# Kernel tuning notes

Measured on AMD Instinct MI355X. Metric: run time of the kernel, lower is better.

The kernel has to match this reference:

```python
import jax, jax.numpy as jnp
import numpy as np

D_MODEL = 384; D_INNER = 768; D_STATE = 64; D_CONV = 4
HEADDIM = 48; NHEADS = 16; NLAYERS = 2
VOCAB = 4104  # 4098 (4096 6-mers + PAD/UNK) padded to multiple of 8
B, L = 32, 512
D_IN_PROJ = 2 * D_INNER + 2 * D_STATE + NHEADS  # 1664
CONV_DIM = D_INNER + 2 * D_STATE  # 896
N_ORDER, N_FAMILY, N_GENUS, N_SPECIES = 60, 427, 14216, 23964


def _layernorm(x, w, b, eps=1e-5):
    mu = jnp.mean(x, -1, keepdims=True)
    var = jnp.mean((x - mu) ** 2, -1, keepdims=True)
    return (x - mu) * jax.lax.rsqrt(var + eps) * w + b


def _mamba2(h, W_in, cw, cb, dtb, alog, d_skip, gw, W_out):
    b, l, _ = h.shape
    zxbcdt = h @ W_in                                  # (b,l,1664)
    z = zxbcdt[..., :D_INNER]
    xBC = zxbcdt[..., D_INNER:D_INNER + CONV_DIM]
    dt = zxbcdt[..., -NHEADS:]
    # causal depthwise conv1d (kernel D_CONV) + silu
    xp = jnp.pad(xBC, ((0, 0), (D_CONV - 1, 0), (0, 0)))
    conv = cb + sum(xp[:, k:k + l, :] * cw[:, k] for k in range(D_CONV))
    xBC = jax.nn.silu(conv)
    x = xBC[..., :D_INNER].reshape(b, l, NHEADS, HEADDIM)
    Bm = xBC[..., D_INNER:D_INNER + D_STATE]           # (b,l,n) ngroups=1
    Cm = xBC[..., D_INNER + D_STATE:]
    dt = jax.nn.softplus(dt + dtb)                     # (b,l,h)
    dA = jnp.exp(dt * (-jnp.exp(alog)))                # per-head scalar decay
    tm = lambda a: jnp.swapaxes(a, 0, 1)               # time-major for scan

    def step(state, inp):
        xt, dtt, dAt, Bt, Ct = inp                     # (b,h,p),(b,h),(b,h),(b,n),(b,n)
        state = state * dAt[:, :, None, None] + jnp.einsum('bhp,bn->bhpn', dtt[..., None] * xt, Bt)
        return state, jnp.einsum('bhpn,bn->bhp', state, Ct)

    state0 = jnp.zeros((b, NHEADS, HEADDIM, D_STATE), h.dtype)
    _, ys = jax.lax.scan(step, state0, (tm(x), tm(dt), tm(dA), tm(Bm), tm(Cm)))
    y = tm(ys) + d_skip[None, None, :, None] * x       # D skip per head
    y = y.reshape(b, l, D_INNER) * jax.nn.silu(z)      # gate
    y = y * jax.lax.rsqrt(jnp.mean(y * y, -1, keepdims=True) + 1e-5) * gw  # gated RMSNorm
    return y @ W_out


def setup_inputs():
    key = jax.random.key(0)
    ks = jax.random.split(key, 16)
    nrm = lambda k, s, sc=0.02: jax.random.normal(k, s, jnp.float32) * sc
    return {
        'tokens': jax.random.randint(ks[0], (B, L), 0, VOCAB),
        'emb': nrm(ks[1], (VOCAB, D_MODEL)),
        'ln_w': jnp.ones((NLAYERS, D_MODEL)), 'ln_b': jnp.zeros((NLAYERS, D_MODEL)),
        'in_proj_w': nrm(ks[2], (NLAYERS, D_MODEL, D_IN_PROJ)),
        'conv_w': nrm(ks[3], (NLAYERS, CONV_DIM, D_CONV), 0.1),
        'conv_b': jnp.zeros((NLAYERS, CONV_DIM)),
        'dt_bias': nrm(ks[4], (NLAYERS, NHEADS), 0.5),
        'A_log': jnp.log(jax.random.uniform(ks[5], (NLAYERS, NHEADS), minval=1.0, maxval=16.0)),
        'D': jnp.ones((NLAYERS, NHEADS)),
        'gnorm_w': jnp.ones((NLAYERS, D_INNER)),
        'out_proj_w': nrm(ks[6], (NLAYERS, D_INNER, D_MODEL)),
        'normf_w': jnp.ones((D_MODEL,)), 'normf_b': jnp.zeros((D_MODEL,)),
        'proj_ln_w': jnp.ones((D_MODEL,)), 'proj_ln_b': jnp.zeros((D_MODEL,)),
        'order_w': nrm(ks[7], (D_MODEL, N_ORDER)), 'order_b': jnp.zeros((N_ORDER,)),
        'family_w': nrm(ks[8], (D_MODEL, N_FAMILY)), 'family_b': jnp.zeros((N_FAMILY,)),
        'genus_w': nrm(ks[9], (D_MODEL, N_GENUS)), 'genus_b': jnp.zeros((N_GENUS,)),
        'species_w': nrm(ks[10], (D_MODEL, N_SPECIES)), 'species_b': jnp.zeros((N_SPECIES,)),
    }


def reference(tokens, emb, ln_w, ln_b, in_proj_w, conv_w, conv_b, dt_bias, A_log, D, gnorm_w, out_proj_w, normf_w, normf_b, proj_ln_w, proj_ln_b, order_w, order_b, family_w, family_b, genus_w, genus_b, species_w, species_b):
    resid = emb[tokens]                                # (B,L,d), embed dropout off (eval)
    for l in range(NLAYERS):                           # pre-norm residual blocks
        h = _layernorm(resid, ln_w[l], ln_b[l])
        resid = resid + _mamba2(h, in_proj_w[l], conv_w[l], conv_b[l], dt_bias[l], A_log[l], D[l], gnorm_w[l], out_proj_w[l])
    h = _layernorm(resid, normf_w, normf_b)            # norm_f -> hidden states
    feat = _layernorm(h.mean(axis=1), proj_ln_w, proj_ln_b)  # mean pool + shared LN (dropout eval)
    return jnp.concatenate([feat @ order_w + order_b,
                            feat @ family_w + family_b,
                            feat @ genus_w + genus_b,
                            feat @ species_w + species_b], axis=-1)
```

## Files before the change

kernel.cpp:

```cpp
#include <hip/hip_runtime.h>
#include <hip/hip_bf16.h>
#include <cmath>


#define B_SZ 32
#define L_SZ 512
#define DMODEL 384
#define DINNER 768
#define DSTATE 64
#define HEADDIM 48
#define NHEADS 16
#define DINPROJ 1680
#define CONVDIM 896
#define ROWS (B_SZ * L_SZ)
#define OUT_STRIDE 38667
#define NCH 8
#define CHL (L_SZ / NCH)
#define N1PAD 1792
#define BCOFF 1536

typedef __hip_bfloat16 bf16;
typedef unsigned short u16;
typedef __attribute__((ext_vector_type(8))) short bfrag;
typedef __attribute__((ext_vector_type(4))) float ffrag;

union BU { uint4 u; bfrag f; };

__device__ __forceinline__ float ldw(const void* p, size_t i, bool isb) {
    if (isb) return __bfloat162float(((const bf16*)p)[i]);
    else     return ((const float*)p)[i];
}

__device__ __forceinline__ short f2bs(float f) {
    unsigned u = __float_as_uint(f);
    u = u + 0x7FFFu + ((u >> 16) & 1u);
    return (short)(u >> 16);
}
__device__ __forceinline__ unsigned pk2(float a, float b) {
    return ((unsigned)(u16)f2bs(a)) | (((unsigned)(u16)f2bs(b)) << 16);
}
__device__ __forceinline__ float blo(unsigned u) { return __uint_as_float(u << 16); }
__device__ __forceinline__ float bhi(unsigned u) { return __uint_as_float(u & 0xFFFF0000u); }

__device__ __forceinline__ void gl2lds16(const void* g, void* l) {
    __builtin_amdgcn_global_load_lds(
        (const __attribute__((address_space(1))) void*)g,
        (__attribute__((address_space(3))) void*)l, 16, 0, 0);
}

__device__ __forceinline__ float* send_f(float* zxd, int s, int off) {
    int seg = off / 768, rem = off - seg * 768;
    return zxd + (size_t)(4 * s + seg) * DINPROJ + DINNER + rem;
}
__device__ __forceinline__ float4* send_q(float* zxd, int s, int off4) {
    return (float4*)send_f(zxd, s, off4);
}

__global__ void detect_kernel(const void* __restrict__ ln_w, int* __restrict__ flag) {
    unsigned u = *(const unsigned*)ln_w;
    *flag = (u == 0x3F800000u) ? 0 : 1;
}

__global__ void embed_kernel(const int* __restrict__ tok,
                             const void* __restrict__ emb,
                             float* __restrict__ resid,
                             const int* __restrict__ dflag) {
    bool isb = (*dflag != 0);
    int r = blockIdx.x, d = threadIdx.x;
    resid[(size_t)r * DMODEL + d] = ldw(emb, (size_t)tok[r] * DMODEL + d, isb);
}

__global__ void layernorm_off(const float* __restrict__ x,
                              const void* __restrict__ w,
                              const void* __restrict__ b, long off,
                              void* __restrict__ out, int D, int obf,
                              const int* __restrict__ dflag) {
    bool isb = (*dflag != 0);
    int row = blockIdx.x, lane = threadIdx.x;
    const float* xr = x + (size_t)row * D;
    float s = 0.f, s2 = 0.f;
    for (int d = lane; d < D; d += 64) { float v = xr[d]; s += v; s2 += v * v; }
    #pragma unroll
    for (int o = 32; o; o >>= 1) { s += __shfl_xor(s, o); s2 += __shfl_xor(s2, o); }
    float mu = s / D;
    float var = s2 / D - mu * mu;
    float rinv = rsqrtf(var + 1e-5f);
    for (int d = lane; d < D; d += 64) {
        float v = (xr[d] - mu) * rinv * ldw(w, off + d, isb) + ldw(b, off + d, isb);
        if (obf) ((u16*)out)[(size_t)row * D + d] = (u16)f2bs(v);
        else     ((float*)out)[(size_t)row * D + d] = v;
    }
}

__global__ void transpose_w(const void* __restrict__ W, long woff,
                            int K, int N, u16* __restrict__ WT, int NT,
                            const int* __restrict__ dflag) {
    bool isb = (*dflag != 0);
    __shared__ float t[64][65];
    int n0 = blockIdx.x * 64, k0 = blockIdx.y * 64;
    for (int i = threadIdx.x; i < 4096; i += 256) {
        int kk = i >> 6, nn = i & 63;
        int gk = k0 + kk, gn = n0 + nn;
        float v = (gn < N && gk < K) ? ldw(W, woff + (size_t)gk * N + gn, isb) : 0.f;
        t[nn][kk] = v;
    }
    __syncthreads();
    for (int i = threadIdx.x; i < 4096; i += 256) {
        int nn = i >> 6, kk = i & 63;
        int gn = n0 + nn, gk = k0 + kk;
        if (gn < NT && gk < K)
            WT[(size_t)gn * K + gk] = (u16)f2bs(t[nn][kk]);
    }
}

__global__ __launch_bounds__(256)
void gemm128(const u16* __restrict__ A, int lda,
             const u16* __restrict__ BT, int ldb,
             float* __restrict__ C, int ldc,
             const float* __restrict__ Cadd,
             int N, int K) {
    __shared__ u16 As[128 * 64];
    __shared__ u16 Bs[128 * 64];
    const int tid = threadIdx.x, lane = tid & 63, w = tid >> 6;
    const int bm = blockIdx.y * 128, bn = blockIdx.x * 128;
    const int wr = w >> 1, wc = w & 1;
    ffrag acc[4][4];
    #pragma unroll
    for (int i = 0; i < 4; ++i)
        #pragma unroll
        for (int j = 0; j < 4; ++j) acc[i][j] = 0.f;

    const int sr = lane >> 3;
    const int swz = (((lane & 7) ^ sr) << 4) >> 1;
    const u16* Asrc = A + (size_t)bm * lda + swz;
    const u16* Bsrc = BT + (size_t)bn * ldb + swz;

    for (int k0 = 0; k0 < K; k0 += 64) {
        #pragma unroll
        for (int i = 0; i < 4; ++i) {
            int r = w * 32 + i * 8 + sr;
            gl2lds16(Asrc + (size_t)r * lda + k0, &As[(w * 32 + i * 8) * 64]);
            gl2lds16(Bsrc + (size_t)r * ldb + k0, &Bs[(w * 32 + i * 8) * 64]);
        }
        __syncthreads();
        #pragma unroll
        for (int ks = 0; ks < 2; ++ks) {
            bfrag af[4], bf[4];
            #pragma unroll
            for (int mi = 0; mi < 4; ++mi) {
                int rr = wr * 64 + mi * 16 + (lane & 15);
                int byte = (rr * 128 + ks * 64 + (lane >> 4) * 16) ^ ((rr & 7) << 4);
                af[mi] = *(const bfrag*)&As[byte >> 1];
            }
            #pragma unroll
            for (int ni = 0; ni < 4; ++ni) {
                int rr = wc * 64 + ni * 16 + (lane & 15);
                int byte = (rr * 128 + ks * 64 + (lane >> 4) * 16) ^ ((rr & 7) << 4);
                bf[ni] = *(const bfrag*)&Bs[byte >> 1];
            }
            #pragma unroll
            for (int mi = 0; mi < 4; ++mi)
                #pragma unroll
                for (int ni = 0; ni < 4; ++ni)
                    acc[mi][ni] = __builtin_amdgcn_mfma_f32_16x16x32_bf16(
                        af[mi], bf[ni], acc[mi][ni], 0, 0, 0);
        }
        __syncthreads();
    }
    int col = lane & 15, r0 = (lane >> 4) * 4;
    #pragma unroll
    for (int mi = 0; mi < 4; ++mi)
        #pragma unroll
        for (int ni = 0; ni < 4; ++ni) {
            int gn = bn + wc * 64 + ni * 16 + col;
            if (gn < N) {
                #pragma unroll
                for (int r = 0; r < 4; ++r) {
                    int gm = bm + wr * 64 + mi * 16 + r0 + r;
                    size_t idx = (size_t)gm * ldc + gn;
                    float v = acc[mi][ni][r];
                    if (Cadd) v += Cadd[idx];
                    C[idx] = v;
                }
            }
        }
}

__global__ void conv_silu_off(const float* __restrict__ zx,
                              const void* __restrict__ cw,
                              const void* __restrict__ cb,
                              long cwoff, long cboff,
                              float* __restrict__ out,
                              const int* __restrict__ dflag) {
    bool isb = (*dflag != 0);
    int c = blockIdx.x * 128 + threadIdx.x;
    int r = blockIdx.y;
    int l = r & (L_SZ - 1);
    float acc = ldw(cb, cboff + c, isb);
    #pragma unroll
    for (int k = 0; k < 4; ++k) {
        int lsrc = l + k - 3;
        if (lsrc >= 0)
            acc += zx[(size_t)(r + k - 3) * DINPROJ + DINNER + c] *
                   ldw(cw, cwoff + c * 4 + k, isb);
    }
    out[(size_t)r * CONVDIM + c] = acc / (1.f + expf(-acc));
}

__global__ __launch_bounds__(256)
void xpose(const float* __restrict__ cbuf, u16* __restrict__ xT) {
    int slot = blockIdx.x, tid = threadIdx.x;
    const float* src = cbuf + (size_t)slot * 64 * CONVDIM;
    u16* dst = xT + (size_t)slot * 49152;
    for (int it = 0; it < 24; ++it) {
        int p = (it % 3) * 256 + tid;
        int tg = it / 3;
        const float* s0 = src + (size_t)(tg * 8) * CONVDIM + p;
        uint4 pk;
        pk.x = pk2(s0[0],           s0[CONVDIM]);
        pk.y = pk2(s0[2 * CONVDIM], s0[3 * CONVDIM]);
        pk.z = pk2(s0[4 * CONVDIM], s0[5 * CONVDIM]);
        pk.w = pk2(s0[6 * CONVDIM], s0[7 * CONVDIM]);
        *(uint4*)(dst + tg * 6144 + p * 8) = pk;
    }
}

__global__ void dt_off(float* __restrict__ zx,
                       const float* __restrict__ convb,
                       const void* __restrict__ dtb,
                       long hoff,
                       float* __restrict__ dtout,
                       const int* __restrict__ dflag) {
    bool isb = (*dflag != 0);
    int idx = blockIdx.x * 256 + threadIdx.x;
    int r = idx >> 4, h = idx & 15;
    float x = zx[(size_t)r * DINPROJ + (DINPROJ - NHEADS) + h] + ldw(dtb, hoff + h, isb);
    float sp = (x > 20.f) ? x : log1pf(expf(x));
    dtout[idx] = sp;
    const float* cv = convb + (size_t)r * CONVDIM + DINNER + h * 8;
    float4 v0 = *(const float4*)cv;
    float4 v1 = *(const float4*)(cv + 4);
    uint4 pk;
    pk.x = pk2(v0.x, v0.y);
    pk.y = pk2(v0.z, v0.w);
    pk.z = pk2(v1.x, v1.y);
    pk.w = pk2(v1.z, v1.w);
    *(uint4*)((u16*)(zx + (size_t)r * DINPROJ + BCOFF) + h * 8) = pk;
}


__global__ __launch_bounds__(512)
void scan_p1(const float* __restrict__ dtg,
             const void* __restrict__ alog, long hoff,
             const u16* __restrict__ xT,
             float* __restrict__ zxd, float* __restrict__ Pbuf,
             const int* __restrict__ dflag) {
    bool isb = (*dflag != 0);
    int c = blockIdx.x & (NCH - 1);
    int hg = (blockIdx.x >> 3) & 1;
    int b = blockIdx.x >> 4;
    int lane = threadIdx.x & 63;
    int wv = threadIdx.x >> 6;
    int h = hg * 8 + wv;
    int slotC = b * NCH + c;
    int slotS = (b << 7) | (h << 3) | c;
    __shared__ __align__(16) u16 BT[64][72];
    __shared__ __align__(16) float La[8][64];
    __shared__ __align__(16) float Dt[8][64];
    #pragma unroll
    for (int it = 0; it < 8; ++it) {
        int idx = it * 512 + threadIdx.x;
        int t = idx >> 6, n = idx & 63;
        BT[n][t] = *((const u16*)(zxd + (size_t)(slotC * 64 + t) * DINPROJ + BCOFF) + n);
    }
    float dtv = dtg[((size_t)slotC * 64 + lane) * NHEADS + h];
    float A = expf(ldw(alog, hoff + h, isb));
    float cs = dtv;
    #pragma unroll
    for (int o = 1; o < 64; o <<= 1) { float v = __shfl_up(cs, o); if (lane >= o) cs += v; }
    La[wv][lane] = -A * cs;
    Dt[wv][lane] = dtv;
    __syncthreads();
    float la63 = La[wv][63];
    ffrag acc[3][4];
    #pragma unroll
    for (int i = 0; i < 3; ++i)
        #pragma unroll
        for (int j = 0; j < 4; ++j) acc[i][j] = 0.f;
    #pragma unroll
    for (int ks = 0; ks < 2; ++ks) {
        int t0 = ks * 32 + (lane >> 4) * 8;
        float4 lA = *(const float4*)&La[wv][t0];
        float4 lB = *(const float4*)&La[wv][t0 + 4];
        float4 dA4 = *(const float4*)&Dt[wv][t0];
        float4 dB4 = *(const float4*)&Dt[wv][t0 + 4];
        float v0 = expf(la63 - lA.x) * dA4.x;
        float v1 = expf(la63 - lA.y) * dA4.y;
        float v2 = expf(la63 - lA.z) * dA4.z;
        float v3 = expf(la63 - lA.w) * dA4.w;
        float v4 = expf(la63 - lB.x) * dB4.x;
        float v5 = expf(la63 - lB.y) * dB4.y;
        float v6 = expf(la63 - lB.z) * dB4.z;
        float v7 = expf(la63 - lB.w) * dB4.w;
        BU xv[3];
        #pragma unroll
        for (int ni = 0; ni < 3; ++ni) {
            int p = h * 48 + (lane & 15) + 16 * ni;
            uint4 raw = *(const uint4*)(xT + (size_t)slotC * 49152 + (t0 >> 3) * 6144 + p * 8);
            xv[ni].u.x = pk2(blo(raw.x) * v0, bhi(raw.x) * v1);
            xv[ni].u.y = pk2(blo(raw.y) * v2, bhi(raw.y) * v3);
            xv[ni].u.z = pk2(blo(raw.z) * v4, bhi(raw.z) * v5);
            xv[ni].u.w = pk2(blo(raw.w) * v6, bhi(raw.w) * v7);
        }
        #pragma unroll
        for (int nj = 0; nj < 4; ++nj) {
            bfrag bt = *(const bfrag*)&BT[(lane & 15) + 16 * nj][t0];
            #pragma unroll
            for (int mi = 0; mi < 3; ++mi)
                acc[mi][nj] = __builtin_amdgcn_mfma_f32_16x16x32_bf16(
                    xv[mi].f, bt, acc[mi][nj], 0, 0, 0);
        }
    }
    #pragma unroll
    for (int mi = 0; mi < 3; ++mi)
        #pragma unroll
        for (int nj = 0; nj < 4; ++nj)
            #pragma unroll
            for (int r = 0; r < 4; ++r) {
                int p = 16 * mi + (lane >> 4) * 4 + r;
                int n = 16 * nj + (lane & 15);
                *send_f(zxd, slotS, p * 64 + n) = acc[mi][nj][r];
            }
    if (lane == 0) Pbuf[slotS] = expf(la63);
}

__global__ void scan_p2(float* __restrict__ zxd, const float* __restrict__ Pbuf) {
    int bh = blockIdx.x;
    int lane = threadIdx.x;
    float4 S[12];
    #pragma unroll
    for (int q = 0; q < 12; ++q) S[q] = make_float4(0.f, 0.f, 0.f, 0.f);
    for (int c = 0; c < NCH - 1; ++c) {
        int s = bh * NCH + c;
        float P = Pbuf[s];
        #pragma unroll
        for (int q = 0; q < 12; ++q) {
            float4* p = send_q(zxd, s, 4 * lane + 256 * q);
            float4 L = *p;
            S[q].x = S[q].x * P + L.x;
            S[q].y = S[q].y * P + L.y;
            S[q].z = S[q].z * P + L.z;
            S[q].w = S[q].w * P + L.w;
            *p = S[q];
        }
    }
}

__global__ __launch_bounds__(512)
void scan_p3(float* __restrict__ convb,
             const float* __restrict__ dtg,
             const void* __restrict__ alog,
             const void* __restrict__ Dsk, long hoff,
             const u16* __restrict__ xT,
             float* __restrict__ zxd,
             const int* __restrict__ dflag) {
    bool isb = (*dflag != 0);
    int c = blockIdx.x & (NCH - 1);
    int hg = (blockIdx.x >> 3) & 1;
    int b = blockIdx.x >> 4;
    int lane = threadIdx.x & 63;
    int wv = threadIdx.x >> 6;
    int h = hg * 8 + wv;
    int slotC = b * NCH + c;
    int slotS = (b << 7) | (h << 3) | c;
    __shared__ __align__(16) u16 Bl[64][72];
    __shared__ __align__(16) u16 Cl[64][72];
    __shared__ __align__(16) float Gl[64][68];
    __shared__ __align__(16) float La[8][64];
    __shared__ __align__(16) float Dt[8][64];
    #pragma unroll
    for (int it = 0; it < 2; ++it) {
        int idx = it * 512 + threadIdx.x;
        int r = idx >> 4, c8 = (idx & 15) * 8;
        uint4 v = *(const uint4*)((const u16*)(zxd + (size_t)(slotC * 64 + r) * DINPROJ + BCOFF) + c8);
        if (c8 < 64) *(uint4*)&Bl[r][c8] = v;
        else         *(uint4*)&Cl[r][c8 - 64] = v;
    }
    float dtv = dtg[((size_t)slotC * 64 + lane) * NHEADS + h];
    float A = expf(ldw(alog, hoff + h, isb));
    float cs = dtv;
    #pragma unroll
    for (int o = 1; o < 64; o <<= 1) { float v = __shfl_up(cs, o); if (lane >= o) cs += v; }
    La[wv][lane] = -A * cs;
    Dt[wv][lane] = dtv;
    __syncthreads();
    if (wv < 4) {
        ffrag g[4];
        #pragma unroll
        for (int j = 0; j < 4; ++j) g[j] = 0.f;
        #pragma unroll
        for (int ks = 0; ks < 2; ++ks) {
            int k0 = ks * 32 + (lane >> 4) * 8;
            bfrag af = *(const bfrag*)&Cl[wv * 16 + (lane & 15)][k0];
            #pragma unroll
            for (int nj = 0; nj < 4; ++nj) {
                bfrag bf = *(const bfrag*)&Bl[(lane & 15) + 16 * nj][k0];
                g[nj] = __builtin_amdgcn_mfma_f32_16x16x32_bf16(af, bf, g[nj], 0, 0, 0);
            }
        }
        #pragma unroll
        for (int nj = 0; nj < 4; ++nj)
            #pragma unroll
            for (int r = 0; r < 4; ++r)
                Gl[wv * 16 + (lane >> 4) * 4 + r][16 * nj + (lane & 15)] = g[nj][r];
    }
    __syncthreads();
    float dskip = ldw(Dsk, hoff + h, isb);
    BU xf[3][2];
    #pragma unroll
    for (int ks = 0; ks < 2; ++ks) {
        int tg = ks * 4 + (lane >> 4);
        #pragma unroll
        for (int ni = 0; ni < 3; ++ni) {
            int p = h * 48 + (lane & 15) + 16 * ni;
            xf[ni][ks].u = *(const uint4*)(xT + (size_t)slotC * 49152 + tg * 6144 + p * 8);
        }
    }
    ffrag aY[4][3];
    #pragma unroll
    for (int i = 0; i < 4; ++i)
        #pragma unroll
        for (int j = 0; j < 3; ++j) aY[i][j] = 0.f;
    #pragma unroll
    for (int ks = 0; ks < 2; ++ks) {
        int t0 = ks * 32 + (lane >> 4) * 8;
        float4 lA = *(const float4*)&La[wv][t0];
        float4 lB = *(const float4*)&La[wv][t0 + 4];
        float4 dA4 = *(const float4*)&Dt[wv][t0];
        float4 dB4 = *(const float4*)&Dt[wv][t0 + 4];
        #pragma unroll
        for (int mi = 0; mi < 4; ++mi) {
            int tloc = (lane & 15) + 16 * mi;
            float lat = La[wv][tloc];
            float4 g0 = *(const float4*)&Gl[tloc][t0];
            float4 g1 = *(const float4*)&Gl[tloc][t0 + 4];
            float m0 = (t0 + 0 <= tloc) ? expf(lat - lA.x) * dA4.x * g0.x : 0.f;
            float m1 = (t0 + 1 <= tloc) ? expf(lat - lA.y) * dA4.y * g0.y : 0.f;
            float m2 = (t0 + 2 <= tloc) ? expf(lat - lA.z) * dA4.z * g0.z : 0.f;
            float m3 = (t0 + 3 <= tloc) ? expf(lat - lA.w) * dA4.w * g0.w : 0.f;
            float m4 = (t0 + 4 <= tloc) ? expf(lat - lB.x) * dB4.x * g1.x : 0.f;
            float m5 = (t0 + 5 <= tloc) ? expf(lat - lB.y) * dB4.y * g1.y : 0.f;
            float m6 = (t0 + 6 <= tloc) ? expf(lat - lB.z) * dB4.z * g1.z : 0.f;
            float m7 = (t0 + 7 <= tloc) ? expf(lat - lB.w) * dB4.w * g1.w : 0.f;
            BU mf;
            mf.u.x = pk2(m0, m1); mf.u.y = pk2(m2, m3);
            mf.u.z = pk2(m4, m5); mf.u.w = pk2(m6, m7);
            #pragma unroll
            for (int ni = 0; ni < 3; ++ni)
                aY[mi][ni] = __builtin_amdgcn_mfma_f32_16x16x32_bf16(
                    mf.f, xf[ni][ks].f, aY[mi][ni], 0, 0, 0);
        }
    }
    if (c > 0) {
        int sprev = slotS - 1;
        #pragma unroll
        for (int ks = 0; ks < 2; ++ks) {
            int n0 = ks * 32 + (lane >> 4) * 8;
            BU s0[3];
            #pragma unroll
            for (int ni = 0; ni < 3; ++ni) {
                int p = (lane & 15) + 16 * ni;
                const float* sp = send_f(zxd, sprev, p * 64 + n0);
                float4 sa = *(const float4*)sp;
                float4 sb = *(const float4*)(sp + 4);
                s0[ni].u.x = pk2(sa.x, sa.y); s0[ni].u.y = pk2(sa.z, sa.w);
                s0[ni].u.z = pk2(sb.x, sb.y); s0[ni].u.w = pk2(sb.z, sb.w);
            }
            #pragma unroll
            for (int mi = 0; mi < 4; ++mi) {
                int tloc = (lane & 15) + 16 * mi;
                float u = expf(La[wv][tloc]);
                BU crU; crU.f = *(const bfrag*)&Cl[tloc][n0];
                BU csc;
                csc.u.x = pk2(blo(crU.u.x) * u, bhi(crU.u.x) * u);
                csc.u.y = pk2(blo(crU.u.y) * u, bhi(crU.u.y) * u);
                csc.u.z = pk2(blo(crU.u.z) * u, bhi(crU.u.z) * u);
                csc.u.w = pk2(blo(crU.u.w) * u, bhi(crU.u.w) * u);
                #pragma unroll
                for (int ni = 0; ni < 3; ++ni)
                    aY[mi][ni] = __builtin_amdgcn_mfma_f32_16x16x32_bf16(
                        csc.f, s0[ni].f, aY[mi][ni], 0, 0, 0);
            }
        }
    }
    #pragma unroll
    for (int mi = 0; mi < 4; ++mi)
        #pragma unroll
        for (int ni = 0; ni < 3; ++ni)
            #pragma unroll
            for (int r = 0; r < 4; ++r) {
                int t = 16 * mi + (lane >> 4) * 4 + r;
                size_t idx = (size_t)(slotC * 64 + t) * CONVDIM + h * 48 + 16 * ni + (lane & 15);
                float x = convb[idx];
                convb[idx] = aY[mi][ni][r] + dskip * x;
            }
}

__global__ void gated_off(float* __restrict__ y,
                          const float* __restrict__ zx,
                          const void* __restrict__ gw, long goff,
                          const int* __restrict__ dflag) {
    bool isb = (*dflag != 0);
    int row = blockIdx.x, tid = threadIdx.x;
    float* yr = y + (size_t)row * CONVDIM;
    const float* zr = zx + (size_t)row * DINPROJ;
    float g[3], s2 = 0.f;
    #pragma unroll
    for (int i = 0; i < 3; ++i) {
        int d = tid + 256 * i;
        float z = zr[d];
        float sz = z / (1.f + expf(-z));
        float v = yr[d] * sz;
        g[i] = v; s2 += v * v;
    }
    #pragma unroll
    for (int o = 32; o; o >>= 1) s2 += __shfl_xor(s2, o);
    __shared__ float red[4];
    if ((tid & 63) == 0) red[tid >> 6] = s2;
    __syncthreads();
    s2 = red[0] + red[1] + red[2] + red[3];
    float rinv = rsqrtf(s2 / (float)DINNER + 1e-5f);
    u16* yb = (u16*)yr;
    #pragma unroll
    for (int i = 0; i < 3; ++i) {
        int d = tid + 256 * i;
        yb[d] = (u16)f2bs(g[i] * rinv * ldw(gw, goff + d, isb));
    }
}

__global__ void pool_part(const float* __restrict__ h, float* __restrict__ part) {
    int b = blockIdx.x, g = blockIdx.y, d = threadIdx.x;
    const float* hp = h + ((size_t)b * L_SZ + g * 64) * DMODEL + d;
    float s = 0.f;
    #pragma unroll 8
    for (int l = 0; l < 64; ++l) s += hp[(size_t)l * DMODEL];
    part[((size_t)b * 8 + g) * DMODEL + d] = s;
}
__global__ void pool_final(const float* __restrict__ part, float* __restrict__ feat0) {
    int b = blockIdx.x, d = threadIdx.x;
    float s = 0.f;
    #pragma unroll
    for (int g = 0; g < 8; ++g) s += part[((size_t)b * 8 + g) * DMODEL + d];
    feat0[b * DMODEL + d] = s * (1.f / L_SZ);
}

__global__ __launch_bounds__(256)
void heads_all(const float* __restrict__ feat,
               const void* __restrict__ Wo, const void* __restrict__ bo,
               const void* __restrict__ Wf, const void* __restrict__ bf_,
               const void* __restrict__ Wg, const void* __restrict__ bg,
               const void* __restrict__ Ws, const void* __restrict__ bs,
               float* __restrict__ out, const int* __restrict__ dflag) {
    bool isb = (*dflag != 0);
    __shared__ __align__(16) float sfT[DMODEL * B_SZ];
    for (int i = threadIdx.x; i < DMODEL * B_SZ; i += 256) {
        int b = i & 31, k = i >> 5;
        sfT[i] = feat[b * DMODEL + k];
    }
    __syncthreads();
    int j = blockIdx.x * 256 + threadIdx.x;
    if (j >= OUT_STRIDE) return;
    const void* W; const void* bias; int N, jl;
    if (j < 60)        { W = Wo; bias = bo;  N = 60;    jl = j; }
    else if (j < 487)  { W = Wf; bias = bf_; N = 427;   jl = j - 60; }
    else if (j < 14703){ W = Wg; bias = bg;  N = 14216; jl = j - 487; }
    else               { W = Ws; bias = bs;  N = 23964; jl = j - 14703; }
    float acc[32];
    #pragma unroll
    for (int b = 0; b < 32; ++b) acc[b] = 0.f;
    for (int k = 0; k < DMODEL; ++k) {
        float w = ldw(W, (size_t)k * N + jl, isb);
        const float4* frow = (const float4*)&sfT[k * 32];
        #pragma unroll
        for (int q = 0; q < 8; ++q) {
            float4 f = frow[q];
            acc[4*q + 0] += f.x * w;
            acc[4*q + 1] += f.y * w;
            acc[4*q + 2] += f.z * w;
            acc[4*q + 3] += f.w * w;
        }
    }
    float bv = ldw(bias, jl, isb);
    #pragma unroll
    for (int b = 0; b < 32; ++b)
        out[(size_t)b * OUT_STRIDE + j] = acc[b] + bv;
}

extern "C" void kernel_launch(void* const* d_in, const int* in_sizes, int n_in,
                              void* d_out, int out_size, void* d_ws, size_t ws_size,
                              hipStream_t stream) {
    const int*  tokens   = (const int*)d_in[0];
    const void* emb      = d_in[1];
    const void* ln_w     = d_in[2];
    const void* ln_b     = d_in[3];
    const void* in_proj  = d_in[4];
    const void* conv_w   = d_in[5];
    const void* conv_b   = d_in[6];
    const void* dt_bias  = d_in[7];
    const void* A_log    = d_in[8];
    const void* Dp       = d_in[9];
    const void* gnorm_w  = d_in[10];
    const void* out_proj = d_in[11];
    const void* normf_w  = d_in[12];
    const void* normf_b  = d_in[13];
    const void* pln_w    = d_in[14];
    const void* pln_b    = d_in[15];
    const void* order_w  = d_in[16];
    const void* order_b  = d_in[17];
    const void* family_w = d_in[18];
    const void* family_b = d_in[19];
    const void* genus_w  = d_in[20];
    const void* genus_b  = d_in[21];
    const void* species_w= d_in[22];
    const void* species_b= d_in[23];
    float* out = (float*)d_out;

    float* ws    = (float*)d_ws;
    float* resid = ws;
    float* hbuf  = resid + (size_t)ROWS * DMODEL;
    float* zx    = hbuf  + (size_t)ROWS * DMODEL;
    float* convb = zx    + (size_t)ROWS * DINPROJ;
    float* dtb_  = convb + (size_t)ROWS * CONVDIM;
    float* dAb   = dtb_  + (size_t)ROWS * NHEADS;
    float* feat0 = dAb   + (size_t)ROWS * NHEADS;
    float* feat  = feat0 + (size_t)B_SZ * DMODEL;
    float* Pbuf  = feat  + (size_t)B_SZ * DMODEL;
    int*   dflag = (int*)(Pbuf + 4096);
    u16*   W1T   = (u16*)(Pbuf + 4096 + 16);
    u16*   W2T   = W1T + (size_t)2 * N1PAD * DMODEL;
    float* ppart = zx;
    u16*   xT    = (u16*)hbuf;

    detect_kernel<<<1, 1, 0, stream>>>(ln_w, dflag);
    embed_kernel<<<ROWS, DMODEL, 0, stream>>>(tokens, emb, resid, dflag);

    for (int l = 0; l < 2; ++l) {
        transpose_w<<<dim3(N1PAD / 64, DMODEL / 64), 256, 0, stream>>>(
            in_proj, (long)l * DMODEL * DINPROJ, DMODEL, DINPROJ,
            W1T + (size_t)l * N1PAD * DMODEL, N1PAD, dflag);
        transpose_w<<<dim3(DMODEL / 64, DINNER / 64), 256, 0, stream>>>(
            out_proj, (long)l * DINNER * DMODEL, DINNER, DMODEL,
            W2T + (size_t)l * DMODEL * DINNER, DMODEL, dflag);
    }

    for (int l = 0; l < 2; ++l) {
        layernorm_off<<<ROWS, 64, 0, stream>>>(resid, ln_w, ln_b,
            (long)l * DMODEL, hbuf, DMODEL, 1, dflag);
        gemm128<<<dim3(N1PAD / 128, ROWS / 128), 256, 0, stream>>>(
            (const u16*)hbuf, DMODEL,
            W1T + (size_t)l * N1PAD * DMODEL, DMODEL,
            zx, DINPROJ, nullptr, DINPROJ, DMODEL);
        conv_silu_off<<<dim3(7, ROWS), 128, 0, stream>>>(
            zx, conv_w, conv_b, (long)l * CONVDIM * 4, (long)l * CONVDIM,
            convb, dflag);
        xpose<<<B_SZ * NCH, 256, 0, stream>>>(convb, xT);
        dt_off<<<(ROWS * NHEADS) / 256, 256, 0, stream>>>(
            zx, convb, dt_bias, (long)l * NHEADS, dtb_, dflag);
        scan_p1<<<B_SZ * 2 * NCH, 512, 0, stream>>>(dtb_, A_log,
            (long)l * NHEADS, xT, zx, Pbuf, dflag);
        scan_p2<<<B_SZ * NHEADS, 64, 0, stream>>>(zx, Pbuf);
        scan_p3<<<B_SZ * 2 * NCH, 512, 0, stream>>>(convb, dtb_, A_log, Dp,
            (long)l * NHEADS, xT, zx, dflag);
        gated_off<<<ROWS, 256, 0, stream>>>(convb, zx, gnorm_w,
            (long)l * DINNER, dflag);
        gemm128<<<dim3(DMODEL / 128, ROWS / 128), 256, 0, stream>>>(
            (const u16*)convb, CONVDIM * 2,
            W2T + (size_t)l * DMODEL * DINNER, DINNER,
            resid, DMODEL, resid, DMODEL, DINNER);
    }

    layernorm_off<<<ROWS, 64, 0, stream>>>(resid, normf_w, normf_b, 0L,
                                           hbuf, DMODEL, 0, dflag);
    pool_part<<<dim3(B_SZ, 8), DMODEL, 0, stream>>>(hbuf, ppart);
    pool_final<<<B_SZ, DMODEL, 0, stream>>>(ppart, feat0);
    layernorm_off<<<B_SZ, 64, 0, stream>>>(feat0, pln_w, pln_b, 0L,
                                           feat, DMODEL, 0, dflag);

    heads_all<<<(OUT_STRIDE + 255) / 256, 256, 0, stream>>>(
        feat, order_w, order_b, family_w, family_b,
        genus_w, genus_b, species_w, species_b, out, dflag);
}
```

Measured before the change: 913.5 us.

## Run classifier heads through bf16 MFMA gemm with transposed padded weights

Replaces the scalar fp32 heads kernel with the existing MFMA gemm. The head weights are transposed and converted to bf16 into a workspace buffer, the features are padded to 128 rows, and the biases are concatenated and added in the gemm epilogue. The aim is to move the head matmul onto matrix cores. The cost is extra transpose passes over about 15M weights, 96 wasted padding rows per tile, and lower precision.

```diff
diff --git a/kernel.cpp b/kernel.cpp
--- a/kernel.cpp
+++ b/kernel.cpp
@@ -14,6 +14,7 @@
 #define CONVDIM 896
 #define ROWS (B_SZ * L_SZ)
 #define OUT_STRIDE 38667
+#define NOUTPAD 38784
 #define NCH 8
 #define CHL (L_SZ / NCH)
 #define N1PAD 1792
@@ -118,7 +119,8 @@
              const u16* __restrict__ BT, int ldb,
              float* __restrict__ C, int ldc,
              const float* __restrict__ Cadd,
-             int N, int K) {
+             int M, int N, int K,
+             const float* __restrict__ bias) {
     __shared__ u16 As[128 * 64];
     __shared__ u16 Bs[128 * 64];
     const int tid = threadIdx.x, lane = tid & 63, w = tid >> 6;
@@ -174,13 +176,16 @@
         for (int ni = 0; ni < 4; ++ni) {
             int gn = bn + wc * 64 + ni * 16 + col;
             if (gn < N) {
+                float bv = bias ? bias[gn] : 0.f;
                 #pragma unroll
                 for (int r = 0; r < 4; ++r) {
                     int gm = bm + wr * 64 + mi * 16 + r0 + r;
-                    size_t idx = (size_t)gm * ldc + gn;
-                    float v = acc[mi][ni][r];
-                    if (Cadd) v += Cadd[idx];
-                    C[idx] = v;
+                    if (gm < M) {
+                        size_t idx = (size_t)gm * ldc + gn;
+                        float v = acc[mi][ni][r] + bv;
+                        if (Cadd) v += Cadd[idx];
+                        C[idx] = v;
+                    }
                 }
             }
         }
@@ -554,46 +559,26 @@
     feat0[b * DMODEL + d] = s * (1.f / L_SZ);
 }
 
-__global__ __launch_bounds__(256)
-void heads_all(const float* __restrict__ feat,
-               const void* __restrict__ Wo, const void* __restrict__ bo,
-               const void* __restrict__ Wf, const void* __restrict__ bf_,
-               const void* __restrict__ Wg, const void* __restrict__ bg,
-               const void* __restrict__ Ws, const void* __restrict__ bs,
-               float* __restrict__ out, const int* __restrict__ dflag) {
-    bool isb = (*dflag != 0);
-    __shared__ __align__(16) float sfT[DMODEL * B_SZ];
-    for (int i = threadIdx.x; i < DMODEL * B_SZ; i += 256) {
-        int b = i & 31, k = i >> 5;
-        sfT[i] = feat[b * DMODEL + k];
-    }
-    __syncthreads();
+__global__ void biascat(const void* __restrict__ bo, const void* __restrict__ bf_,
+                        const void* __restrict__ bg, const void* __restrict__ bs,
+                        float* __restrict__ biasAll, const int* __restrict__ dflag) {
+    bool isb = (*dflag != 0);
     int j = blockIdx.x * 256 + threadIdx.x;
     if (j >= OUT_STRIDE) return;
-    const void* W; const void* bias; int N, jl;
-    if (j < 60)        { W = Wo; bias = bo;  N = 60;    jl = j; }
-    else if (j < 487)  { W = Wf; bias = bf_; N = 427;   jl = j - 60; }
-    else if (j < 14703){ W = Wg; bias = bg;  N = 14216; jl = j - 487; }
-    else               { W = Ws; bias = bs;  N = 23964; jl = j - 14703; }
-    float acc[32];
-    #pragma unroll
-    for (int b = 0; b < 32; ++b) acc[b] = 0.f;
-    for (int k = 0; k < DMODEL; ++k) {
-        float w = ldw(W, (size_t)k * N + jl, isb);
-        const float4* frow = (const float4*)&sfT[k * 32];
-        #pragma unroll
-        for (int q = 0; q < 8; ++q) {
-            float4 f = frow[q];
-            acc[4*q + 0] += f.x * w;
-            acc[4*q + 1] += f.y * w;
-            acc[4*q + 2] += f.z * w;
-            acc[4*q + 3] += f.w * w;
-        }
-    }
-    float bv = ldw(bias, jl, isb);
-    #pragma unroll
-    for (int b = 0; b < 32; ++b)
-        out[(size_t)b * OUT_STRIDE + j] = acc[b] + bv;
+    float v;
+    if (j < 60)        v = ldw(bo, j, isb);
+    else if (j < 487)  v = ldw(bf_, j - 60, isb);
+    else if (j < 14703) v = ldw(bg, j - 487, isb);
+    else               v = ldw(bs, j - 14703, isb);
+    biasAll[j] = v;
+}
+__global__ void pad_feat(const float* __restrict__ feat, u16* __restrict__ featp) {
+    int r = blockIdx.x, d = threadIdx.x;
+    featp[r * DMODEL + d] = (r < B_SZ) ? (u16)f2bs(feat[r * DMODEL + d]) : (u16)0;
+}
+__global__ void zero_wpad(u16* __restrict__ WhT) {
+    int r = blockIdx.x, d = threadIdx.x;
+    WhT[(size_t)(OUT_STRIDE + r) * DMODEL + d] = 0;
 }
 
 extern "C" void kernel_launch(void* const* d_in, const int* in_sizes, int n_in,
@@ -640,9 +625,14 @@
     u16*   W2T   = W1T + (size_t)2 * N1PAD * DMODEL;
     float* ppart = zx;
     u16*   xT    = (u16*)hbuf;
+    u16*   WhT   = (u16*)(zx + 262144);
+    u16*   featp = (u16*)dAb;
+    float* biasAll = (float*)(featp + 128 * DMODEL);
 
     detect_kernel<<<1, 1, 0, stream>>>(ln_w, dflag);
     embed_kernel<<<ROWS, DMODEL, 0, stream>>>(tokens, emb, resid, dflag);
+    biascat<<<(OUT_STRIDE + 255) / 256, 256, 0, stream>>>(
+        order_b, family_b, genus_b, species_b, biasAll, dflag);
 
     for (int l = 0; l < 2; ++l) {
         transpose_w<<<dim3(N1PAD / 64, DMODEL / 64), 256, 0, stream>>>(
@@ -659,7 +649,7 @@
         gemm128<<<dim3(N1PAD / 128, ROWS / 128), 256, 0, stream>>>(
             (const u16*)hbuf, DMODEL,
             W1T + (size_t)l * N1PAD * DMODEL, DMODEL,
-            zx, DINPROJ, nullptr, DINPROJ, DMODEL);
+            zx, DINPROJ, nullptr, ROWS, DINPROJ, DMODEL, nullptr);
         conv_silu_off<<<dim3(7, ROWS), 128, 0, stream>>>(
             zx, conv_w, conv_b, (long)l * CONVDIM * 4, (long)l * CONVDIM,
             convb, dflag);
@@ -676,8 +666,18 @@
         gemm128<<<dim3(DMODEL / 128, ROWS / 128), 256, 0, stream>>>(
             (const u16*)convb, CONVDIM * 2,
             W2T + (size_t)l * DMODEL * DINNER, DINNER,
-            resid, DMODEL, resid, DMODEL, DINNER);
-    }
+            resid, DMODEL, resid, ROWS, DMODEL, DINNER, nullptr);
+    }
+
+    transpose_w<<<dim3(1, 6), 256, 0, stream>>>(
+        order_w, 0L, DMODEL, 60, WhT, 60, dflag);
+    transpose_w<<<dim3(7, 6), 256, 0, stream>>>(
+        family_w, 0L, DMODEL, 427, WhT + (size_t)60 * DMODEL, 427, dflag);
+    transpose_w<<<dim3(223, 6), 256, 0, stream>>>(
+        genus_w, 0L, DMODEL, 14216, WhT + (size_t)487 * DMODEL, 14216, dflag);
+    transpose_w<<<dim3(375, 6), 256, 0, stream>>>(
+        species_w, 0L, DMODEL, 23964, WhT + (size_t)14703 * DMODEL, 23964, dflag);
+    zero_wpad<<<NOUTPAD - OUT_STRIDE, DMODEL, 0, stream>>>(WhT);
 
     layernorm_off<<<ROWS, 64, 0, stream>>>(resid, normf_w, normf_b, 0L,
                                            hbuf, DMODEL, 0, dflag);
@@ -685,8 +685,9 @@
     pool_final<<<B_SZ, DMODEL, 0, stream>>>(ppart, feat0);
     layernorm_off<<<B_SZ, 64, 0, stream>>>(feat0, pln_w, pln_b, 0L,
                                            feat, DMODEL, 0, dflag);
-
-    heads_all<<<(OUT_STRIDE + 255) / 256, 256, 0, stream>>>(
-        feat, order_w, order_b, family_w, family_b,
-        genus_w, genus_b, species_w, species_b, out, dflag);
-}
+    pad_feat<<<128, DMODEL, 0, stream>>>(feat, featp);
+
+    gemm128<<<dim3(NOUTPAD / 128, 1), 256, 0, stream>>>(
+        featp, DMODEL, WhT, DMODEL,
+        out, OUT_STRIDE, nullptr, B_SZ, OUT_STRIDE, DMODEL, biasAll);
+}
```

Result: faster. 893.5 us (-2.2%).
